# Kernel optimization log

Measured on AMD Instinct MI355X. Metric: run time of the kernel, lower is better.

## Reference

```python
import jax, jax.numpy as jnp
import numpy as np

BN_EPS = 1e-5


def maxpool2(x):
    # 2x2 max pool, stride 2: (B,C,H,W) -> (B,C,H//2,W//2)
    B, C, H, W = x.shape
    return x.reshape(B, C, H // 2, 2, W // 2, 2).max(axis=(3, 5))


def setup_inputs() -> dict:
    key = jax.random.key(0)
    ks = jax.random.split(key, 6)
    B, C, H, W = 4, 64, 96, 96   # in_dim = 64
    K, OD = 64, 64               # key_dim, out_dim
    sc = lambda fan: 1.0 / np.sqrt(fan)
    return {
        "c2": jax.random.normal(ks[0], (B, C, H, W), jnp.float32),
        "x": jax.random.normal(ks[1], (B, C, H, W), jnp.float32),
        # edge_att: Conv2d(2C->OD, 1x1, no bias) -> BN -> ReLU -> Conv2d(OD->1, 1x1) -> Sigmoid
        "w_ea1": jax.random.normal(ks[2], (OD, 2 * C), jnp.float32) * sc(2 * C),
        "bn_w": jnp.ones((OD,), jnp.float32),
        "bn_b": jnp.zeros((OD,), jnp.float32),
        "bn_m": jnp.zeros((OD,), jnp.float32),
        "bn_v": jnp.ones((OD,), jnp.float32),
        "w_ea2": jax.random.normal(ks[3], (1, OD), jnp.float32) * sc(OD),
        "b_ea2": jnp.zeros((1,), jnp.float32),
        # query_conv (shared for query AND key in the original forward)
        "w_q": jax.random.normal(ks[4], (K, C), jnp.float32) * sc(C),
        "b_q": jnp.zeros((K,), jnp.float32),
        "gamma": jnp.full((1,), 0.5, jnp.float32),
    }


def reference(c2, x, w_ea1, bn_w, bn_b, bn_m, bn_v, w_ea2, b_ea2, w_q, b_q, gamma):
    xp = maxpool2(x)        # (B,C,Hp,Wp)
    c2p = maxpool2(c2)
    B, C, H, W = x.shape
    Hp, Wp = xp.shape[2], xp.shape[3]

    # edge attention gate on pooled features -> (B,1,Hp,Wp)
    cat = jnp.concatenate([c2p, xp], axis=1)                       # (B,2C,Hp,Wp)
    h = jnp.einsum('oc,bchw->bohw', w_ea1, cat)
    bn_scale = (bn_w / jnp.sqrt(bn_v + BN_EPS))[None, :, None, None]
    h = jax.nn.relu((h - bn_m[None, :, None, None]) * bn_scale + bn_b[None, :, None, None])
    ea = jax.nn.sigmoid(jnp.einsum('oc,bchw->bohw', w_ea2, h) + b_ea2[None, :, None, None])

    # query at full res, key at pooled res (SAME conv weights, as in the source)
    q = jnp.einsum('kc,bchw->bkhw', w_q, x) + b_q[None, :, None, None]    # (B,K,H,W)
    k = jnp.einsum('kc,bchw->bkhw', w_q, xp) + b_q[None, :, None, None]   # (B,K,Hp,Wp)

    pq = q.reshape(B, -1, H * W)        # (B,K,N)
    pk = k.reshape(B, -1, Hp * Wp)      # (B,K,M)
    energy = jnp.einsum('bkn,bkm->bnm', pq, pk)                    # (B,N,M)
    attn = jax.nn.softmax(energy * ea.reshape(B, 1, Hp * Wp), axis=-1)

    v = xp.reshape(B, C, Hp * Wp)                                   # (B,C,M)
    out = jnp.einsum('bcm,bnm->bcn', v, attn).reshape(B, C, H, W)
    return gamma[0] * out + x
```

## Files before the change

### kernel.cpp

```cpp
#include <hip/hip_runtime.h>
#include <stdint.h>

#define B_ 4
#define C_ 64
#define H_ 96
#define W_ 96
#define HP_ 48
#define WP_ 48
#define N_ (H_*W_)
#define M_ (HP_*WP_)
#define KD_ 64
#define OD_ 64
#define BN_EPS 1e-5f
#define LOG2E 1.4426950408889634f
#define SHIFT2 28.853900817779268f
#define QT_ 48
#define QB_ (N_/QT_)

typedef __bf16 bf16_t;
typedef bf16_t bf16x8 __attribute__((ext_vector_type(8)));
typedef bf16_t bf16x4 __attribute__((ext_vector_type(4)));
typedef float f32x4 __attribute__((ext_vector_type(4)));
typedef short short4v __attribute__((ext_vector_type(4)));

static __device__ __forceinline__ unsigned short f2bf(float f) {
    unsigned int u = __builtin_bit_cast(unsigned int, f);
    u += 0x7fffu + ((u >> 16) & 1u);
    return (unsigned short)(u >> 16);
}

static __device__ __forceinline__ f32x4 mfma16_bf16(short4v a, short4v b, f32x4 c) {
#if __has_builtin(__builtin_amdgcn_mfma_f32_16x16x16bf16_1k)
    return __builtin_amdgcn_mfma_f32_16x16x16bf16_1k(a, b, c, 0, 0, 0);
#else
    return c;
#endif
}

__global__ __launch_bounds__(256) void prep_kernel(
    const float* __restrict__ x, const float* __restrict__ c2,
    const float* __restrict__ wq, const float* __restrict__ bq,
    const float* __restrict__ w1, const float* __restrict__ bnw, const float* __restrict__ bnb,
    const float* __restrict__ bnm, const float* __restrict__ bnv,
    const float* __restrict__ w2, const float* __restrict__ b2,
    unsigned short* __restrict__ kb, unsigned short* __restrict__ vb, float* __restrict__ ea) {

    __shared__ float lw1[OD_*2*C_];
    __shared__ float lwq[KD_*C_];
    __shared__ float xs[C_*33];
    __shared__ float c2s[C_*33];
    __shared__ float red[8][32];

    int tid = threadIdx.x;
    int b = blockIdx.x / 72;
    int m0 = (blockIdx.x % 72) * 32;

    for (int i = tid; i < OD_*2*C_; i += 256) lw1[i] = w1[i];
    for (int i = tid; i < KD_*C_; i += 256) lwq[i] = wq[i];
    for (int j = tid; j < 2048; j += 256) {
        int c = j >> 5, p = j & 31;
        int m = m0 + p;
        int hp = m / WP_, wp = m % WP_;
        size_t base = ((size_t)(b*C_ + c)*H_ + 2*hp)*W_ + 2*wp;
        const float* px = x + base;
        float mx = fmaxf(fmaxf(px[0], px[1]), fmaxf(px[W_], px[W_+1]));
        xs[c*33 + p] = mx;
        vb[(size_t)(b*C_ + c)*M_ + m] = f2bf(mx);
        const float* pc = c2 + base;
        c2s[c*33 + p] = fmaxf(fmaxf(pc[0], pc[1]), fmaxf(pc[W_], pc[W_+1]));
    }
    __syncthreads();

    int ml = tid & 31, oz = tid >> 5;
    int m = m0 + ml;

    float h[8] = {0,0,0,0,0,0,0,0};
    for (int c = 0; c < C_; c += 4) {
        float x0 = xs[c*33+ml], x1 = xs[(c+1)*33+ml], x2 = xs[(c+2)*33+ml], x3 = xs[(c+3)*33+ml];
        #pragma unroll
        for (int oi = 0; oi < 8; oi++) {
            const float4 wv = *(const float4*)&lwq[(oz*8 + oi)*C_ + c];
            h[oi] = fmaf(wv.x, x0, fmaf(wv.y, x1, fmaf(wv.z, x2, fmaf(wv.w, x3, h[oi]))));
        }
    }
    unsigned short tmp[8];
    #pragma unroll
    for (int oi = 0; oi < 8; oi++) tmp[oi] = f2bf(h[oi] + bq[oz*8 + oi]);
    *(uint4*)&kb[((size_t)b*M_ + m)*KD_ + oz*8] = *(const uint4*)tmp;

    float g[8] = {0,0,0,0,0,0,0,0};
    for (int c = 0; c < 2*C_; c += 4) {
        const float* srcb = (c < C_) ? &c2s[c*33] : &xs[(c - C_)*33];
        float x0 = srcb[ml], x1 = srcb[33+ml], x2 = srcb[66+ml], x3 = srcb[99+ml];
        #pragma unroll
        for (int oi = 0; oi < 8; oi++) {
            const float4 wv = *(const float4*)&lw1[(oz*8 + oi)*(2*C_) + c];
            g[oi] = fmaf(wv.x, x0, fmaf(wv.y, x1, fmaf(wv.z, x2, fmaf(wv.w, x3, g[oi]))));
        }
    }
    float z = 0.f;
    #pragma unroll
    for (int oi = 0; oi < 8; oi++) {
        int o = oz*8 + oi;
        float sc = bnw[o] * rsqrtf(bnv[o] + BN_EPS);
        float t = (g[oi] - bnm[o]) * sc + bnb[o];
        z += w2[o] * fmaxf(t, 0.f);
    }
    red[oz][ml] = z;
    __syncthreads();
    if (oz == 0) {
        float s = b2[0];
        #pragma unroll
        for (int i = 0; i < 8; i++) s += red[i][ml];
        ea[(size_t)b*M_ + m] = LOG2E / (1.f + __builtin_amdgcn_exp2f(-s * LOG2E));
    }
}

__global__ __launch_bounds__(256) void qk_kernel(const float* __restrict__ in, const float* __restrict__ wq,
    const float* __restrict__ bq, unsigned short* __restrict__ outb) {
    __shared__ float lw[KD_*C_];
    for (int i = threadIdx.x; i < KD_*C_; i += 256) lw[i] = wq[i];
    __syncthreads();
    int ml = threadIdx.x & 31, oz = threadIdx.x >> 5;
    int pg = blockIdx.x * 32 + ml;
    float h[8] = {0,0,0,0,0,0,0,0};
    const float* src = in + ((size_t)(pg / N_))*C_*N_ + (pg % N_);
    for (int c = 0; c < C_; c += 4) {
        float x0 = src[(size_t)c*N_], x1 = src[(size_t)(c+1)*N_];
        float x2 = src[(size_t)(c+2)*N_], x3 = src[(size_t)(c+3)*N_];
        #pragma unroll
        for (int oi = 0; oi < 8; oi++) {
            const float4 wv = *(const float4*)&lw[(oz*8 + oi)*C_ + c];
            h[oi] = fmaf(wv.x, x0, fmaf(wv.y, x1, fmaf(wv.z, x2, fmaf(wv.w, x3, h[oi]))));
        }
    }
    unsigned short tmp[8];
    #pragma unroll
    for (int oi = 0; oi < 8; oi++) tmp[oi] = f2bf(h[oi] + bq[oz*8 + oi]);
    *(uint4*)&outb[(size_t)pg*KD_ + oz*8] = *(const uint4*)tmp;
}

__global__ __launch_bounds__(256, 3) void attn_kernel(
    const unsigned short* __restrict__ qb, const unsigned short* __restrict__ kb,
    const unsigned short* __restrict__ vb, const float* __restrict__ ea,
    const float* __restrict__ x, const float* __restrict__ gamma_p, float* __restrict__ out) {

    __shared__ __align__(16) char smem[36864];

    int tid = threadIdx.x;
    int wave = tid >> 6, lane = tid & 63, quad = lane >> 4, l16 = lane & 15;
    int blk = blockIdx.x;
    int b = (blk & 7) >> 1;
    int n_base = ((blk & 1) * (QB_/2) + (blk >> 3)) * QT_;

    bf16x8 qf[3][2];
    #pragma unroll
    for (int qi = 0; qi < 3; qi++) {
        const unsigned short* qp = qb + ((size_t)b*N_ + n_base + qi*16 + l16)*KD_;
        qf[qi][0] = __builtin_bit_cast(bf16x8, *(const uint4*)(qp + quad*8));
        qf[qi][1] = __builtin_bit_cast(bf16x8, *(const uint4*)(qp + 32 + quad*8));
    }

    f32x4 o2[3][4];
    f32x4 lacc[3];
    #pragma unroll
    for (int qi = 0; qi < 3; qi++) {
        lacc[qi] = (f32x4){0.f,0.f,0.f,0.f};
        #pragma unroll
        for (int ct = 0; ct < 4; ct++) o2[qi][ct] = (f32x4){0.f,0.f,0.f,0.f};
    }
    const short one_bf = (short)0x3F80;
    short4v ones = (short4v){one_bf, one_bf, one_bf, one_bf};

    const unsigned short* kbB = kb + (size_t)b*M_*KD_;
    const unsigned short* vbB = vb + (size_t)b*C_*M_;
    const float* eaB = ea + (size_t)b*M_;

    int r0 = tid >> 3, g8 = (tid & 7) << 3;
    uint4 kA, kB, vA, vB;

    {
        kA = *(const uint4*)(kbB + (size_t)r0*KD_ + g8);
        kB = *(const uint4*)(kbB + (size_t)(r0+32)*KD_ + g8);
        vA = *(const uint4*)(vbB + (size_t)r0*M_ + g8);
        vB = *(const uint4*)(vbB + (size_t)(r0+32)*M_ + g8);
        unsigned short* k0 = (unsigned short*)smem;
        unsigned short* v0 = (unsigned short*)(smem + 9216);
        *(uint4*)(k0 + r0*72 + g8) = kA;
        *(uint4*)(k0 + (r0+32)*72 + g8) = kB;
        *(uint4*)(v0 + r0*72 + g8) = vA;
        *(uint4*)(v0 + (r0+32)*72 + g8) = vB;
    }
    __syncthreads();

    for (int mt = 0; mt < M_/64; mt++) {
        int cur = mt & 1;
        if (mt < M_/64 - 1) {
            int mb = (mt+1) * 64;
            kA = *(const uint4*)(kbB + (size_t)(mb + r0)*KD_ + g8);
            kB = *(const uint4*)(kbB + (size_t)(mb + r0 + 32)*KD_ + g8);
            vA = *(const uint4*)(vbB + (size_t)r0*M_ + mb + g8);
            vB = *(const uint4*)(vbB + (size_t)(r0+32)*M_ + mb + g8);
        }
        unsigned short* kc = (unsigned short*)(smem + cur*18432);
        unsigned short* vc = (unsigned short*)(smem + cur*18432 + 9216);

        f32x4 e4 = *(const f32x4*)(eaB + mt*64 + wave*16 + quad*4);

        bf16x8 kf0 = __builtin_bit_cast(bf16x8, *(const uint4*)(kc + (wave*16 + l16)*72 + quad*8));
        bf16x8 kf1 = __builtin_bit_cast(bf16x8, *(const uint4*)(kc + (wave*16 + l16)*72 + 32 + quad*8));
        short4v va[4];
        #pragma unroll
        for (int ct = 0; ct < 4; ct++)
            va[ct] = *(const short4v*)(vc + (ct*16 + l16)*72 + wave*16 + quad*4);

        f32x4 st[3];
        #pragma unroll
        for (int qi = 0; qi < 3; qi++) {
            f32x4 z = (f32x4){0.f,0.f,0.f,0.f};
            z = __builtin_amdgcn_mfma_f32_16x16x32_bf16(kf0, qf[qi][0], z, 0, 0, 0);
            z = __builtin_amdgcn_mfma_f32_16x16x32_bf16(kf1, qf[qi][1], z, 0, 0, 0);
            st[qi] = z;
        }

        short4v pk[3];
        #pragma unroll
        for (int qi = 0; qi < 3; qi++) {
            f32x4 p;
            p[0] = __builtin_amdgcn_exp2f(fmaf(st[qi][0], e4[0], -SHIFT2));
            p[1] = __builtin_amdgcn_exp2f(fmaf(st[qi][1], e4[1], -SHIFT2));
            p[2] = __builtin_amdgcn_exp2f(fmaf(st[qi][2], e4[2], -SHIFT2));
            p[3] = __builtin_amdgcn_exp2f(fmaf(st[qi][3], e4[3], -SHIFT2));
            pk[qi] = __builtin_bit_cast(short4v, __builtin_convertvector(p, bf16x4));
        }

        #pragma unroll
        for (int ct = 0; ct < 4; ct++)
            #pragma unroll
            for (int qi = 0; qi < 3; qi++)
                o2[qi][ct] = mfma16_bf16(va[ct], pk[qi], o2[qi][ct]);
        #pragma unroll
        for (int qi = 0; qi < 3; qi++)
            lacc[qi] = mfma16_bf16(ones, pk[qi], lacc[qi]);

        if (mt < M_/64 - 1) {
            int nxt = 1 - cur;
            unsigned short* kd = (unsigned short*)(smem + nxt*18432);
            unsigned short* vd = (unsigned short*)(smem + nxt*18432 + 9216);
            *(uint4*)(kd + r0*72 + g8) = kA;
            *(uint4*)(kd + (r0+32)*72 + g8) = kB;
            *(uint4*)(vd + r0*72 + g8) = vA;
            *(uint4*)(vd + (r0+32)*72 + g8) = vB;
        }
        __syncthreads();
    }

    float* o_red0 = (float*)smem;
    float* o_red1 = o_red0 + 48*68;
    float* l_red  = o_red1 + 48*68;

    if (lane < 16) {
        #pragma unroll
        for (int qi = 0; qi < 3; qi++) l_red[wave*48 + qi*16 + l16] = lacc[qi][0];
    }
    if (wave < 2) {
        float* od = (wave == 0) ? o_red0 : o_red1;
        #pragma unroll
        for (int qi = 0; qi < 3; qi++)
            #pragma unroll
            for (int ct = 0; ct < 4; ct++)
                *(f32x4*)&od[(qi*16 + l16)*68 + ct*16 + quad*4] = o2[qi][ct];
    }
    __syncthreads();
    if (wave >= 2) {
        float* od = (wave == 2) ? o_red0 : o_red1;
        #pragma unroll
        for (int qi = 0; qi < 3; qi++)
            #pragma unroll
            for (int ct = 0; ct < 4; ct++) {
                f32x4* p = (f32x4*)&od[(qi*16 + l16)*68 + ct*16 + quad*4];
                *p += o2[qi][ct];
            }
    }
    __syncthreads();
    if (tid < 48) {
        float s = (l_red[tid] + l_red[48 + tid]) + (l_red[96 + tid] + l_red[144 + tid]);
        l_red[tid] = 1.f / s;
    }
    __syncthreads();

    float gmm = gamma_p[0];
    int c = tid >> 2, q4 = tid & 3;
    const float* xrow = x + ((size_t)b*C_ + c)*N_ + n_base;
    float* orow = out + ((size_t)b*C_ + c)*N_ + n_base;
    #pragma unroll
    for (int i = 0; i < 3; i++) {
        int q0 = q4*4 + i*16;
        float4 xv = *(const float4*)(xrow + q0);
        float4 ov;
        float v0 = (o_red0[(q0+0)*68 + c] + o_red1[(q0+0)*68 + c]) * l_red[q0+0];
        float v1 = (o_red0[(q0+1)*68 + c] + o_red1[(q0+1)*68 + c]) * l_red[q0+1];
        float v2 = (o_red0[(q0+2)*68 + c] + o_red1[(q0+2)*68 + c]) * l_red[q0+2];
        float v3 = (o_red0[(q0+3)*68 + c] + o_red1[(q0+3)*68 + c]) * l_red[q0+3];
        ov.x = fmaf(gmm, v0, xv.x);
        ov.y = fmaf(gmm, v1, xv.y);
        ov.z = fmaf(gmm, v2, xv.z);
        ov.w = fmaf(gmm, v3, xv.w);
        *(float4*)(orow + q0) = ov;
    }
}

extern "C" void kernel_launch(void* const* d_in, const int* in_sizes, int n_in,
                              void* d_out, int out_size, void* d_ws, size_t ws_size,
                              hipStream_t stream) {
    const float* c2    = (const float*)d_in[0];
    const float* x     = (const float*)d_in[1];
    const float* w_ea1 = (const float*)d_in[2];
    const float* bn_w  = (const float*)d_in[3];
    const float* bn_b  = (const float*)d_in[4];
    const float* bn_m  = (const float*)d_in[5];
    const float* bn_v  = (const float*)d_in[6];
    const float* w_ea2 = (const float*)d_in[7];
    const float* b_ea2 = (const float*)d_in[8];
    const float* w_q   = (const float*)d_in[9];
    const float* b_q   = (const float*)d_in[10];
    const float* gamma = (const float*)d_in[11];
    float* out = (float*)d_out;

    char* ws = (char*)d_ws;
    float* ea            = (float*)(ws + 0);
    unsigned short* qb   = (unsigned short*)(ws + 36864);
    unsigned short* kb   = (unsigned short*)(ws + 4755456);
    unsigned short* vb   = (unsigned short*)(ws + 5935104);

    prep_kernel<<<dim3((B_*M_)/32), dim3(256), 0, stream>>>(x, c2, w_q, b_q,
        w_ea1, bn_w, bn_b, bn_m, bn_v, w_ea2, b_ea2, kb, vb, ea);
    qk_kernel<<<dim3((B_*N_)/32), dim3(256), 0, stream>>>(x, w_q, b_q, qb);
    attn_kernel<<<dim3(B_*QB_), dim3(256), 0, stream>>>(qb, kb, vb, ea, x, gamma, out);
}
```

Measured before the change: 165.9 us.

## Stage K/V tiles via direct global-to-LDS loads with XOR swizzle and MFMA priority

Replaces the register-staged global->LDS copy of K and V tiles with global_load_lds direct transfers into a double buffer. Padding is dropped in favour of an XOR-swizzled layout to avoid LDS bank conflicts, which also shrinks shared memory. s_setprio hints raise wave priority around MFMA sections. This saves VGPRs and VALU/ds_write traffic. The risk is that it relies on __syncthreads correctly waiting on the asynchronous LDS loads (vmcnt), and falls back to a no-op if the builtin is missing.

```diff
diff --git a/kernel.cpp b/kernel.cpp
--- a/kernel.cpp
+++ b/kernel.cpp
@@ -16,6 +16,7 @@
 #define SHIFT2 28.853900817779268f
 #define QT_ 48
 #define QB_ (N_/QT_)
+#define NT_ (M_/64)
 
 typedef __bf16 bf16_t;
 typedef bf16_t bf16x8 __attribute__((ext_vector_type(8)));
@@ -34,6 +35,25 @@
     return __builtin_amdgcn_mfma_f32_16x16x16bf16_1k(a, b, c, 0, 0, 0);
 #else
     return c;
+#endif
+}
+
+static __device__ __forceinline__ void gl_lds16(const unsigned short* g, unsigned short* l) {
+#if __has_builtin(__builtin_amdgcn_global_load_lds)
+    __builtin_amdgcn_global_load_lds(
+        (const __attribute__((address_space(1))) unsigned int*)(const void*)g,
+        (__attribute__((address_space(3))) unsigned int*)(void*)l, 16, 0, 0);
+#endif
+}
+
+static __device__ __forceinline__ void setprio1() {
+#if __has_builtin(__builtin_amdgcn_s_setprio)
+    __builtin_amdgcn_s_setprio(1);
+#endif
+}
+static __device__ __forceinline__ void setprio0() {
+#if __has_builtin(__builtin_amdgcn_s_setprio)
+    __builtin_amdgcn_s_setprio(0);
 #endif
 }
 
@@ -145,7 +165,7 @@
     const unsigned short* __restrict__ vb, const float* __restrict__ ea,
     const float* __restrict__ x, const float* __restrict__ gamma_p, float* __restrict__ out) {
 
-    __shared__ __align__(16) char smem[36864];
+    __shared__ __align__(16) char smem[32768];
 
     int tid = threadIdx.x;
     int wave = tid >> 6, lane = tid & 63, quad = lane >> 4, l16 = lane & 15;
@@ -176,45 +196,45 @@
     const unsigned short* vbB = vb + (size_t)b*C_*M_;
     const float* eaB = ea + (size_t)b*M_;
 
-    int r0 = tid >> 3, g8 = (tid & 7) << 3;
-    uint4 kA, kB, vA, vB;
-
-    {
-        kA = *(const uint4*)(kbB + (size_t)r0*KD_ + g8);
-        kB = *(const uint4*)(kbB + (size_t)(r0+32)*KD_ + g8);
-        vA = *(const uint4*)(vbB + (size_t)r0*M_ + g8);
-        vB = *(const uint4*)(vbB + (size_t)(r0+32)*M_ + g8);
-        unsigned short* k0 = (unsigned short*)smem;
-        unsigned short* v0 = (unsigned short*)(smem + 9216);
-        *(uint4*)(k0 + r0*72 + g8) = kA;
-        *(uint4*)(k0 + (r0+32)*72 + g8) = kB;
-        *(uint4*)(v0 + r0*72 + g8) = vA;
-        *(uint4*)(v0 + (r0+32)*72 + g8) = vB;
-    }
-    __syncthreads();
-
-    for (int mt = 0; mt < M_/64; mt++) {
+    int srow = tid >> 3;
+    int ksw  = ((tid & 7) ^ (srow & 7)) << 3;
+
+    auto STAGE = [&](int mb, char* kd, char* vd) {
+        unsigned short* kds = (unsigned short*)kd;
+        unsigned short* vds = (unsigned short*)vd;
+        gl_lds16(kbB + (size_t)(mb + srow)*KD_      + ksw, kds + tid*8);
+        gl_lds16(kbB + (size_t)(mb + srow + 32)*KD_ + ksw, kds + 2048 + tid*8);
+        gl_lds16(vbB + (size_t)srow*M_      + mb + ksw, vds + tid*8);
+        gl_lds16(vbB + (size_t)(srow+32)*M_ + mb + ksw, vds + 2048 + tid*8);
+    };
+
+    STAGE(0, smem, smem + 8192);
+    __syncthreads();
+
+    int xsw = l16 & 7;
+
+    for (int mt = 0; mt < NT_; mt++) {
         int cur = mt & 1;
-        if (mt < M_/64 - 1) {
-            int mb = (mt+1) * 64;
-            kA = *(const uint4*)(kbB + (size_t)(mb + r0)*KD_ + g8);
-            kB = *(const uint4*)(kbB + (size_t)(mb + r0 + 32)*KD_ + g8);
-            vA = *(const uint4*)(vbB + (size_t)r0*M_ + mb + g8);
-            vB = *(const uint4*)(vbB + (size_t)(r0+32)*M_ + mb + g8);
-        }
-        unsigned short* kc = (unsigned short*)(smem + cur*18432);
-        unsigned short* vc = (unsigned short*)(smem + cur*18432 + 9216);
+        if (mt < NT_ - 1) {
+            char* nb = smem + (1 - cur)*16384;
+            STAGE((mt+1)*64, nb, nb + 8192);
+        }
+        unsigned short* kc = (unsigned short*)(smem + cur*16384);
+        unsigned short* vc = (unsigned short*)(smem + cur*16384 + 8192);
 
         f32x4 e4 = *(const f32x4*)(eaB + mt*64 + wave*16 + quad*4);
 
-        bf16x8 kf0 = __builtin_bit_cast(bf16x8, *(const uint4*)(kc + (wave*16 + l16)*72 + quad*8));
-        bf16x8 kf1 = __builtin_bit_cast(bf16x8, *(const uint4*)(kc + (wave*16 + l16)*72 + 32 + quad*8));
+        int krow = wave*16 + l16;
+        bf16x8 kf0 = __builtin_bit_cast(bf16x8, *(const uint4*)(kc + krow*KD_ + (((quad  ) ^ xsw) << 3)));
+        bf16x8 kf1 = __builtin_bit_cast(bf16x8, *(const uint4*)(kc + krow*KD_ + (((quad+4) ^ xsw) << 3)));
         short4v va[4];
         #pragma unroll
         for (int ct = 0; ct < 4; ct++)
-            va[ct] = *(const short4v*)(vc + (ct*16 + l16)*72 + wave*16 + quad*4);
+            va[ct] = *(const short4v*)(vc + (ct*16 + l16)*64
+                        + (((wave*2 + (quad>>1)) ^ xsw) << 3) + (quad&1)*4);
 
         f32x4 st[3];
+        setprio1();
         #pragma unroll
         for (int qi = 0; qi < 3; qi++) {
             f32x4 z = (f32x4){0.f,0.f,0.f,0.f};
@@ -222,6 +242,7 @@
             z = __builtin_amdgcn_mfma_f32_16x16x32_bf16(kf1, qf[qi][1], z, 0, 0, 0);
             st[qi] = z;
         }
+        setprio0();
 
         short4v pk[3];
         #pragma unroll
@@ -234,6 +255,7 @@
             pk[qi] = __builtin_bit_cast(short4v, __builtin_convertvector(p, bf16x4));
         }
 
+        setprio1();
         #pragma unroll
         for (int ct = 0; ct < 4; ct++)
             #pragma unroll
@@ -242,16 +264,8 @@
         #pragma unroll
         for (int qi = 0; qi < 3; qi++)
             lacc[qi] = mfma16_bf16(ones, pk[qi], lacc[qi]);
-
-        if (mt < M_/64 - 1) {
-            int nxt = 1 - cur;
-            unsigned short* kd = (unsigned short*)(smem + nxt*18432);
-            unsigned short* vd = (unsigned short*)(smem + nxt*18432 + 9216);
-            *(uint4*)(kd + r0*72 + g8) = kA;
-            *(uint4*)(kd + (r0+32)*72 + g8) = kB;
-            *(uint4*)(vd + r0*72 + g8) = vA;
-            *(uint4*)(vd + (r0+32)*72 + g8) = vB;
-        }
+        setprio0();
+
         __syncthreads();
     }
 
```

Measured after the change: 162.5 us. 2.0% less time.
